# Performance work log

Measured on AMD Instinct MI355X. Metric: run time of the kernel, lower is better.

Reference implementation:

```python
import jax, jax.numpy as jnp
import numpy as np

IN_FEATURES = 4096
OUT_FEATURES = 4096
CODESZ = 4
CB_SIZE = 256


def fwht(x):
    """Fast Walsh-Hadamard transform over the last dim (power of 2), unnormalized."""
    shape = x.shape
    n = shape[-1]
    x = x.reshape(-1, n)
    h = 1
    while h < n:  # log2(n) fixed iterations
        x = x.reshape(x.shape[0], -1, 2, h)
        a = x[:, :, 0:1, :]
        b = x[:, :, 1:2, :]
        x = jnp.concatenate([a + b, a - b], axis=2)
        h *= 2
    return x.reshape(shape)


def setup_inputs() -> dict:
    key = jax.random.key(0)
    k1, k2, k3, k4, k5, k6 = jax.random.split(key, 6)
    inp = {
        "input": jax.random.normal(k1, (4, 2048, IN_FEATURES), dtype=jnp.float32),
        "SU": jax.random.uniform(k2, (IN_FEATURES,), dtype=jnp.float32),
        "SV": jax.random.uniform(k3, (OUT_FEATURES,), dtype=jnp.float32),
        "cb": jax.random.normal(k4, (CB_SIZE, CODESZ), dtype=jnp.float32),
        "Qidxs": jax.random.randint(k5, (OUT_FEATURES, IN_FEATURES // CODESZ), 0, CB_SIZE, dtype=jnp.int32),
        "Wscale": jnp.ones((1,), dtype=jnp.float32),
        "bias": jax.random.normal(k6, (OUT_FEATURES,), dtype=jnp.float32),
    }
    return inp


def reference(input, SU, SV, cb, Qidxs, Wscale, bias):
    q_in = IN_FEATURES   # power of 2 -> had_left is None, K_left = 1
    q_out = OUT_FEATURES # power of 2 -> had_right is None, K_right = 1
    x = input.reshape(-1, input.shape[-1])          # [T, in]
    x = x * SU                                       # input sign/scale vector
    # matmul_hadUt_cuda: FWHT / sqrt(n) * wscale
    x = fwht(x) * (Wscale[0] / jnp.sqrt(jnp.float32(q_in)))
    # codebook decode + matmul: W [q_out, q_in] from indices
    W = cb[Qidxs].reshape(q_out, q_in)               # gather decode
    out = jnp.einsum('ti,oi->to', x, W)              # [T, q_out]
    # matmul_hadU_cuda on the output side: FWHT / sqrt(n)
    out = fwht(out) / jnp.sqrt(jnp.float32(q_out))
    out = out[..., :OUT_FEATURES]
    out = out * SV
    out = out.reshape(*input.shape[:-1], OUT_FEATURES)
    out = out + bias
    return out
```

## Files before the change

### kernel.cpp

```cpp
#include <hip/hip_runtime.h>
#include <cstdint>


using bf16x8 = __attribute__((ext_vector_type(8))) __bf16;
using f32x4  = __attribute__((ext_vector_type(4))) float;

__device__ __forceinline__ unsigned short f2bf(float f) {
    unsigned int u = __float_as_uint(f);
    unsigned int r = (u + 0x7fffu + ((u >> 16) & 1u)) >> 16;
    return (unsigned short)r;
}

__device__ __forceinline__ void fwht4096(float* row, int t) {
    for (int h = 1; h < 4096; h <<= 1) {
#pragma unroll
        for (int q = 0; q < 8; ++q) {
            int p = t + (q << 8);
            int i = ((p & ~(h - 1)) << 1) | (p & (h - 1));
            float a = row[i];
            float b = row[i + h];
            row[i]     = a + b;
            row[i + h] = a - b;
        }
        __syncthreads();
    }
}

__global__ __launch_bounds__(256) void fwht_in_kernel(const float* __restrict__ inp,
                                                      const float* __restrict__ SU,
                                                      const float* __restrict__ wscale,
                                                      unsigned short* __restrict__ X) {
    __shared__ float row[4096];
    const int t = threadIdx.x;
    const size_t base = (size_t)blockIdx.x * 4096;
    const float4* in4 = (const float4*)(inp + base);
    const float4* su4 = (const float4*)SU;
#pragma unroll
    for (int j = 0; j < 4; ++j) {
        int v = t + (j << 8);
        float4 x = in4[v];
        float4 s = su4[v];
        x.x *= s.x; x.y *= s.y; x.z *= s.z; x.w *= s.w;
        ((float4*)row)[v] = x;
    }
    __syncthreads();
    fwht4096(row, t);
    const float sc = wscale[0] * 0.015625f;
#pragma unroll
    for (int j = 0; j < 2; ++j) {
        int i0 = (t << 3) + (j << 11);
        union { unsigned short us[8]; uint4 v4; } pk;
#pragma unroll
        for (int c = 0; c < 8; ++c) pk.us[c] = f2bf(row[i0 + c] * sc);
        *(uint4*)(X + base + i0) = pk.v4;
    }
}

__global__ __launch_bounds__(256) void decode_kernel(const int* __restrict__ Qidxs,
                                                     const float* __restrict__ cb,
                                                     unsigned short* __restrict__ Wb) {
    __shared__ float4 cbs[256];
    const int t = threadIdx.x;
    cbs[t] = ((const float4*)cb)[t];
    __syncthreads();
    const size_t o = blockIdx.x;
    const int* q = Qidxs + o * 1024;
    ushort4* wrow = (ushort4*)(Wb + o * 4096);
#pragma unroll
    for (int jj = 0; jj < 4; ++jj) {
        int j = t + (jj << 8);
        int idx = q[j];
        float4 v = cbs[idx];
        ushort4 w4;
        w4.x = f2bf(v.x); w4.y = f2bf(v.y); w4.z = f2bf(v.z); w4.w = f2bf(v.w);
        wrow[j] = w4;
    }
}


__device__ __forceinline__ void stage_part(const unsigned short* __restrict__ src,
                                           int grow, int kt,
                                           unsigned short* dst, int tid) {
#pragma unroll
    for (int j = 0; j < 2; ++j) {
        int u = tid + j * 512;
        int r = u >> 3;
        int q = (u & 7) ^ (r & 7);
        const unsigned short* g = src + (size_t)(grow + r) * 4096 + kt + q * 8;
        __builtin_amdgcn_global_load_lds(
            (const __attribute__((address_space(1))) unsigned int*)g,
            (__attribute__((address_space(3))) unsigned int*)((char*)dst + u * 16),
            16, 0, 0);
    }
}

#define VM4 asm volatile("s_waitcnt vmcnt(4)" ::: "memory")
#define VM0 asm volatile("s_waitcnt vmcnt(0)" ::: "memory")

#define PHASE(MQ, NQ, PA, PB, STAGE, VM) do {                                      \
    bf16x8 a0_[4], a1_[4], b0_[2], b1_[2];                                         \
    const char* pA_ = (const char*)(PA);                                           \
    const char* pB_ = (const char*)(PB);                                           \
    _Pragma("unroll")                                                              \
    for (int mf_ = 0; mf_ < 4; ++mf_) {                                            \
        a0_[mf_] = *(const bf16x8*)(pA_ + aRow + mf_ * 4096 + pu0);                \
        a1_[mf_] = *(const bf16x8*)(pA_ + aRow + mf_ * 4096 + pu1);                \
    }                                                                              \
    _Pragma("unroll")                                                              \
    for (int nf_ = 0; nf_ < 2; ++nf_) {                                            \
        b0_[nf_] = *(const bf16x8*)(pB_ + bRow + nf_ * 8192 + pu0);                \
        b1_[nf_] = *(const bf16x8*)(pB_ + bRow + nf_ * 8192 + pu1);                \
    }                                                                              \
    STAGE;                                                                         \
    __builtin_amdgcn_s_barrier();                                                  \
    __builtin_amdgcn_s_setprio(1);                                                 \
    _Pragma("unroll")                                                              \
    for (int mf_ = 0; mf_ < 4; ++mf_) {                                            \
        _Pragma("unroll")                                                          \
        for (int nf_ = 0; nf_ < 2; ++nf_) {                                        \
            acc[(MQ)*4 + mf_][(NQ)*2 + nf_] = __builtin_amdgcn_mfma_f32_16x16x32_bf16( \
                a0_[mf_], b0_[nf_], acc[(MQ)*4 + mf_][(NQ)*2 + nf_], 0, 0, 0);     \
            acc[(MQ)*4 + mf_][(NQ)*2 + nf_] = __builtin_amdgcn_mfma_f32_16x16x32_bf16( \
                a1_[mf_], b1_[nf_], acc[(MQ)*4 + mf_][(NQ)*2 + nf_], 0, 0, 0);     \
        }                                                                          \
    }                                                                              \
    __builtin_amdgcn_s_setprio(0);                                                 \
    VM;                                                                            \
    __builtin_amdgcn_s_barrier();                                                  \
} while (0)

__global__ __launch_bounds__(512, 2) void gemm8_kernel(const unsigned short* __restrict__ X,
                                                       const unsigned short* __restrict__ Wb,
                                                       float* __restrict__ C) {
    __shared__ unsigned short ldsA[2][2][8192];
    __shared__ unsigned short ldsB[2][2][8192];

    const int tid  = threadIdx.x;
    const int lane = tid & 63;
    const int w    = tid >> 6;
    const int wm   = w >> 2;
    const int wn   = w & 3;

    const int bid   = blockIdx.x;
    const int xcd   = bid & 7;
    const int local = bid >> 3;
    const int tm = (xcd >> 1) * 8 + (local >> 3);
    const int tn = (xcd & 1) * 8 + (local & 7);
    const int brow = tm * 256;
    const int bcol = tn * 256;

    const int lr = lane & 15;
    const int lh = lane & 7;
    const int lg = lane >> 4;
    const int aRow = (wm * 16 + lr) * 128;
    const int bRow = (wn * 16 + lr) * 128;
    const int pu0 = (lg ^ lh) * 16;
    const int pu1 = ((4 + lg) ^ lh) * 16;

    f32x4 acc[8][4] = {};

    stage_part(X,  brow,       0,  &ldsA[0][0][0], tid);
    stage_part(Wb, bcol,       0,  &ldsB[0][0][0], tid);
    stage_part(Wb, bcol + 128, 0,  &ldsB[0][1][0], tid);
    stage_part(X,  brow + 128, 0,  &ldsA[0][1][0], tid);
    stage_part(X,  brow,       64, &ldsA[1][0][0], tid);
    stage_part(Wb, bcol,       64, &ldsB[1][0][0], tid);
    VM4;
    __builtin_amdgcn_s_barrier();

    for (int i = 0; i < 31; ++i) {
        const int kt1 = i * 128 + 64;
        const int ktA = i * 128 + 128;
        const int ktB = i * 128 + 192;
        PHASE(0, 0, &ldsA[0][0][0], &ldsB[0][0][0], stage_part(Wb, bcol + 128, kt1, &ldsB[1][1][0], tid), );
        PHASE(0, 1, &ldsA[0][0][0], &ldsB[0][1][0], stage_part(X,  brow + 128, kt1, &ldsA[1][1][0], tid), );
        PHASE(1, 0, &ldsA[0][1][0], &ldsB[0][0][0], stage_part(X,  brow,       ktA, &ldsA[0][0][0], tid), );
        PHASE(1, 1, &ldsA[0][1][0], &ldsB[0][1][0], stage_part(Wb, bcol,       ktA, &ldsB[0][0][0], tid), VM4);
        PHASE(0, 0, &ldsA[1][0][0], &ldsB[1][0][0], stage_part(Wb, bcol + 128, ktA, &ldsB[0][1][0], tid), );
        PHASE(0, 1, &ldsA[1][0][0], &ldsB[1][1][0], stage_part(X,  brow + 128, ktA, &ldsA[0][1][0], tid), );
        PHASE(1, 0, &ldsA[1][1][0], &ldsB[1][0][0], stage_part(X,  brow,       ktB, &ldsA[1][0][0], tid), );
        PHASE(1, 1, &ldsA[1][1][0], &ldsB[1][1][0], stage_part(Wb, bcol,       ktB, &ldsB[1][0][0], tid), VM4);
    }
    {
        const int kt1 = 4032;
        PHASE(0, 0, &ldsA[0][0][0], &ldsB[0][0][0], stage_part(Wb, bcol + 128, kt1, &ldsB[1][1][0], tid), );
        PHASE(0, 1, &ldsA[0][0][0], &ldsB[0][1][0], stage_part(X,  brow + 128, kt1, &ldsA[1][1][0], tid), );
        PHASE(1, 0, &ldsA[0][1][0], &ldsB[0][0][0], , );
        PHASE(1, 1, &ldsA[0][1][0], &ldsB[0][1][0], , VM0);
        PHASE(0, 0, &ldsA[1][0][0], &ldsB[1][0][0], , );
        PHASE(0, 1, &ldsA[1][0][0], &ldsB[1][1][0], , );
        PHASE(1, 0, &ldsA[1][1][0], &ldsB[1][0][0], , );
        PHASE(1, 1, &ldsA[1][1][0], &ldsB[1][1][0], , );
    }

#pragma unroll
    for (int mf = 0; mf < 8; ++mf) {
        int row0 = brow + wm * 16 + mf * 32 + (lane >> 4) * 4;
#pragma unroll
        for (int nf = 0; nf < 4; ++nf) {
            int col = bcol + wn * 16 + nf * 64 + lr;
#pragma unroll
            for (int r = 0; r < 4; ++r)
                C[(size_t)(row0 + r) * 4096 + col] = acc[mf][nf][r];
        }
    }
}

__global__ __launch_bounds__(256) void fwht_out_kernel(float* __restrict__ out,
                                                       const float* __restrict__ SV,
                                                       const float* __restrict__ bias) {
    __shared__ float row[4096];
    const int t = threadIdx.x;
    const size_t base = (size_t)blockIdx.x * 4096;
    float4* o4 = (float4*)(out + base);
#pragma unroll
    for (int j = 0; j < 4; ++j) {
        int v = t + (j << 8);
        ((float4*)row)[v] = o4[v];
    }
    __syncthreads();
    fwht4096(row, t);
    const float4* sv4 = (const float4*)SV;
    const float4* b4  = (const float4*)bias;
#pragma unroll
    for (int j = 0; j < 4; ++j) {
        int v = t + (j << 8);
        float4 x = ((float4*)row)[v];
        float4 s = sv4[v];
        float4 b = b4[v];
        x.x = x.x * (s.x * 0.015625f) + b.x;
        x.y = x.y * (s.y * 0.015625f) + b.y;
        x.z = x.z * (s.z * 0.015625f) + b.z;
        x.w = x.w * (s.w * 0.015625f) + b.w;
        o4[v] = x;
    }
}

extern "C" void kernel_launch(void* const* d_in, const int* in_sizes, int n_in,
                              void* d_out, int out_size, void* d_ws, size_t ws_size,
                              hipStream_t stream) {
    const float* inp    = (const float*)d_in[0];
    const float* SU     = (const float*)d_in[1];
    const float* SV     = (const float*)d_in[2];
    const float* cb     = (const float*)d_in[3];
    const int*   Qidxs  = (const int*)d_in[4];
    const float* Wscale = (const float*)d_in[5];
    const float* bias   = (const float*)d_in[6];
    float* out = (float*)d_out;

    unsigned short* X  = (unsigned short*)d_ws;
    unsigned short* Wb = (unsigned short*)((char*)d_ws + (size_t)8192 * 4096 * 2);

    hipLaunchKernelGGL(fwht_in_kernel, dim3(8192), dim3(256), 0, stream, inp, SU, Wscale, X);
    hipLaunchKernelGGL(decode_kernel,  dim3(4096), dim3(256), 0, stream, Qidxs, cb, Wb);
    hipLaunchKernelGGL(gemm8_kernel,   dim3(512),  dim3(512), 0, stream, X, Wb, out);
    hipLaunchKernelGGL(fwht_out_kernel, dim3(8192), dim3(256), 0, stream, out, SV, bias);
}
```

Measured before the change: 612.4 us.

## Use register radix-16 FWHT with XOR-swizzled LDS and reuse fragments in GEMM

Both FWHT kernels move from 12 barrier-separated radix-2 passes over shared memory to three radix-16 passes. Each pass does a 16-point transform in registers, using an XOR-swizzled layout so the strided accesses avoid bank conflicts. This removes most barriers and shared-memory traffic. The GEMM main loop is also restructured to load A and B fragments once per k-subtile and reuse them across the four quadrant MFMA groups in a snake order, cutting LDS reads at the cost of extra live registers.

```diff
diff --git a/kernel.cpp b/kernel.cpp
--- a/kernel.cpp
+++ b/kernel.cpp
@@ -11,48 +11,81 @@
     return (unsigned short)r;
 }
 
-__device__ __forceinline__ void fwht4096(float* row, int t) {
-    for (int h = 1; h < 4096; h <<= 1) {
-#pragma unroll
-        for (int q = 0; q < 8; ++q) {
-            int p = t + (q << 8);
-            int i = ((p & ~(h - 1)) << 1) | (p & (h - 1));
-            float a = row[i];
-            float b = row[i + h];
-            row[i]     = a + b;
-            row[i + h] = a - b;
+__device__ __forceinline__ void h16(float v[16]) {
+#pragma unroll
+    for (int h = 1; h < 16; h <<= 1) {
+#pragma unroll
+        for (int g = 0; g < 16; g += (h << 1)) {
+#pragma unroll
+            for (int k = g; k < g + h; ++k) {
+                float x = v[k], y = v[k + h];
+                v[k] = x + y; v[k + h] = x - y;
+            }
         }
-        __syncthreads();
-    }
-}
+    }
+}
+
 
 __global__ __launch_bounds__(256) void fwht_in_kernel(const float* __restrict__ inp,
                                                       const float* __restrict__ SU,
                                                       const float* __restrict__ wscale,
                                                       unsigned short* __restrict__ X) {
-    __shared__ float row[4096];
+    __shared__ float s[4096];
     const int t = threadIdx.x;
     const size_t base = (size_t)blockIdx.x * 4096;
     const float4* in4 = (const float4*)(inp + base);
     const float4* su4 = (const float4*)SU;
 #pragma unroll
     for (int j = 0; j < 4; ++j) {
-        int v = t + (j << 8);
+        const int v = t + (j << 8);
         float4 x = in4[v];
-        float4 s = su4[v];
-        x.x *= s.x; x.y *= s.y; x.z *= s.z; x.w *= s.w;
-        ((float4*)row)[v] = x;
-    }
-    __syncthreads();
-    fwht4096(row, t);
+        float4 u = su4[v];
+        x.x *= u.x; x.y *= u.y; x.z *= u.z; x.w *= u.w;
+        const int a = v >> 6, b = (v >> 2) & 15, c0 = (v & 3) << 2;
+        float* row = s + a * 256 + ((b ^ a) << 4);
+        row[(c0 + 0) ^ b] = x.x; row[(c0 + 1) ^ b] = x.y;
+        row[(c0 + 2) ^ b] = x.z; row[(c0 + 3) ^ b] = x.w;
+    }
+    __syncthreads();
+    float v[16];
+    {
+        const int a = t >> 4, b = t & 15;
+        float* row = s + a * 256 + ((b ^ a) << 4);
+#pragma unroll
+        for (int c = 0; c < 16; ++c) v[c] = row[c ^ b];
+        h16(v);
+#pragma unroll
+        for (int c = 0; c < 16; ++c) row[c ^ b] = v[c];
+    }
+    __syncthreads();
+    {
+        const int a = t >> 4, c = t & 15;
+#pragma unroll
+        for (int b = 0; b < 16; ++b) v[b] = s[a * 256 + ((b ^ a) << 4) + (c ^ b)];
+        h16(v);
+#pragma unroll
+        for (int b = 0; b < 16; ++b) s[a * 256 + ((b ^ a) << 4) + (c ^ b)] = v[b];
+    }
+    __syncthreads();
+    {
+        const int b = t >> 4, c = t & 15;
+#pragma unroll
+        for (int a = 0; a < 16; ++a) v[a] = s[a * 256 + ((b ^ a) << 4) + (c ^ b)];
+        h16(v);
+#pragma unroll
+        for (int a = 0; a < 16; ++a) s[a * 256 + ((b ^ a) << 4) + (c ^ b)] = v[a];
+    }
+    __syncthreads();
     const float sc = wscale[0] * 0.015625f;
 #pragma unroll
-    for (int j = 0; j < 2; ++j) {
-        int i0 = (t << 3) + (j << 11);
-        union { unsigned short us[8]; uint4 v4; } pk;
-#pragma unroll
-        for (int c = 0; c < 8; ++c) pk.us[c] = f2bf(row[i0 + c] * sc);
-        *(uint4*)(X + base + i0) = pk.v4;
+    for (int p = 0; p < 2; ++p) {
+        const int i0 = (p << 11) + (t << 3);
+        const int a = i0 >> 8, b = (i0 >> 4) & 15, c0 = i0 & 15;
+        const float* row = s + a * 256 + ((b ^ a) << 4);
+        union { unsigned short us[8]; uint4 q; } pk;
+#pragma unroll
+        for (int z = 0; z < 8; ++z) pk.us[z] = f2bf(row[(c0 + z) ^ b] * sc);
+        *(uint4*)(X + base + i0) = pk.q;
     }
 }
 
@@ -97,36 +130,42 @@
 #define VM4 asm volatile("s_waitcnt vmcnt(4)" ::: "memory")
 #define VM0 asm volatile("s_waitcnt vmcnt(0)" ::: "memory")
 
-#define PHASE(MQ, NQ, PA, PB, STAGE, VM) do {                                      \
-    bf16x8 a0_[4], a1_[4], b0_[2], b1_[2];                                         \
+#define RD_A(HOFF) do { _Pragma("unroll")                                          \
+    for (int m_ = 0; m_ < 4; ++m_) {                                               \
+        Ak0[m_] = *(const bf16x8*)(pA_ + (HOFF) + aRow + m_ * 4096 + pu0);         \
+        Ak1[m_] = *(const bf16x8*)(pA_ + (HOFF) + aRow + m_ * 4096 + pu1);         \
+    } } while (0)
+
+#define RD_B(D0, D1, HOFF) do { _Pragma("unroll")                                  \
+    for (int n_ = 0; n_ < 2; ++n_) {                                               \
+        D0[n_] = *(const bf16x8*)(pB_ + (HOFF) + bRow + n_ * 8192 + pu0);          \
+        D1[n_] = *(const bf16x8*)(pB_ + (HOFF) + bRow + n_ * 8192 + pu1);          \
+    } } while (0)
+
+#define MMQ(MQ, NQ, Bk0, Bk1) do {                                                 \
+    __builtin_amdgcn_s_setprio(1);                                                 \
+    _Pragma("unroll")                                                              \
+    for (int m_ = 0; m_ < 4; ++m_) { _Pragma("unroll")                             \
+        for (int n_ = 0; n_ < 2; ++n_) {                                           \
+            acc[(MQ)*4+m_][(NQ)*2+n_] = __builtin_amdgcn_mfma_f32_16x16x32_bf16(   \
+                Ak0[m_], Bk0[n_], acc[(MQ)*4+m_][(NQ)*2+n_], 0, 0, 0);             \
+            acc[(MQ)*4+m_][(NQ)*2+n_] = __builtin_amdgcn_mfma_f32_16x16x32_bf16(   \
+                Ak1[m_], Bk1[n_], acc[(MQ)*4+m_][(NQ)*2+n_], 0, 0, 0);             \
+        } }                                                                        \
+    __builtin_amdgcn_s_setprio(0); } while (0)
+
+#define KTILE(PA, PB, ST1, ST2, ST3, ST4, VM_) do {                                \
     const char* pA_ = (const char*)(PA);                                           \
     const char* pB_ = (const char*)(PB);                                           \
-    _Pragma("unroll")                                                              \
-    for (int mf_ = 0; mf_ < 4; ++mf_) {                                            \
-        a0_[mf_] = *(const bf16x8*)(pA_ + aRow + mf_ * 4096 + pu0);                \
-        a1_[mf_] = *(const bf16x8*)(pA_ + aRow + mf_ * 4096 + pu1);                \
-    }                                                                              \
-    _Pragma("unroll")                                                              \
-    for (int nf_ = 0; nf_ < 2; ++nf_) {                                            \
-        b0_[nf_] = *(const bf16x8*)(pB_ + bRow + nf_ * 8192 + pu0);                \
-        b1_[nf_] = *(const bf16x8*)(pB_ + bRow + nf_ * 8192 + pu1);                \
-    }                                                                              \
-    STAGE;                                                                         \
-    __builtin_amdgcn_s_barrier();                                                  \
-    __builtin_amdgcn_s_setprio(1);                                                 \
-    _Pragma("unroll")                                                              \
-    for (int mf_ = 0; mf_ < 4; ++mf_) {                                            \
-        _Pragma("unroll")                                                          \
-        for (int nf_ = 0; nf_ < 2; ++nf_) {                                        \
-            acc[(MQ)*4 + mf_][(NQ)*2 + nf_] = __builtin_amdgcn_mfma_f32_16x16x32_bf16( \
-                a0_[mf_], b0_[nf_], acc[(MQ)*4 + mf_][(NQ)*2 + nf_], 0, 0, 0);     \
-            acc[(MQ)*4 + mf_][(NQ)*2 + nf_] = __builtin_amdgcn_mfma_f32_16x16x32_bf16( \
-                a1_[mf_], b1_[nf_], acc[(MQ)*4 + mf_][(NQ)*2 + nf_], 0, 0, 0);     \
-        }                                                                          \
-    }                                                                              \
-    __builtin_amdgcn_s_setprio(0);                                                 \
-    VM;                                                                            \
-    __builtin_amdgcn_s_barrier();                                                  \
+    bf16x8 Ak0[4], Ak1[4], B0k0[2], B0k1[2], B1k0[2], B1k1[2];                     \
+    RD_A(0); RD_B(B0k0, B0k1, 0); ST1; __builtin_amdgcn_s_barrier();               \
+    MMQ(0, 0, B0k0, B0k1); __builtin_amdgcn_s_barrier();                           \
+    RD_B(B1k0, B1k1, 16384); ST2; __builtin_amdgcn_s_barrier();                    \
+    MMQ(0, 1, B1k0, B1k1); __builtin_amdgcn_s_barrier();                           \
+    RD_A(16384); ST3; __builtin_amdgcn_s_barrier();                                \
+    MMQ(1, 1, B1k0, B1k1); __builtin_amdgcn_s_barrier();                           \
+    ST4; __builtin_amdgcn_s_barrier();                                             \
+    MMQ(1, 0, B0k0, B0k1); VM_; __builtin_amdgcn_s_barrier();                      \
 } while (0)
 
 __global__ __launch_bounds__(512, 2) void gemm8_kernel(const unsigned short* __restrict__ X,
@@ -172,25 +211,24 @@
         const int kt1 = i * 128 + 64;
         const int ktA = i * 128 + 128;
         const int ktB = i * 128 + 192;
-        PHASE(0, 0, &ldsA[0][0][0], &ldsB[0][0][0], stage_part(Wb, bcol + 128, kt1, &ldsB[1][1][0], tid), );
-        PHASE(0, 1, &ldsA[0][0][0], &ldsB[0][1][0], stage_part(X,  brow + 128, kt1, &ldsA[1][1][0], tid), );
-        PHASE(1, 0, &ldsA[0][1][0], &ldsB[0][0][0], stage_part(X,  brow,       ktA, &ldsA[0][0][0], tid), );
-        PHASE(1, 1, &ldsA[0][1][0], &ldsB[0][1][0], stage_part(Wb, bcol,       ktA, &ldsB[0][0][0], tid), VM4);
-        PHASE(0, 0, &ldsA[1][0][0], &ldsB[1][0][0], stage_part(Wb, bcol + 128, ktA, &ldsB[0][1][0], tid), );
-        PHASE(0, 1, &ldsA[1][0][0], &ldsB[1][1][0], stage_part(X,  brow + 128, ktA, &ldsA[0][1][0], tid), );
-        PHASE(1, 0, &ldsA[1][1][0], &ldsB[1][0][0], stage_part(X,  brow,       ktB, &ldsA[1][0][0], tid), );
-        PHASE(1, 1, &ldsA[1][1][0], &ldsB[1][1][0], stage_part(Wb, bcol,       ktB, &ldsB[1][0][0], tid), VM4);
-    }
-    {
-        const int kt1 = 4032;
-        PHASE(0, 0, &ldsA[0][0][0], &ldsB[0][0][0], stage_part(Wb, bcol + 128, kt1, &ldsB[1][1][0], tid), );
-        PHASE(0, 1, &ldsA[0][0][0], &ldsB[0][1][0], stage_part(X,  brow + 128, kt1, &ldsA[1][1][0], tid), );
-        PHASE(1, 0, &ldsA[0][1][0], &ldsB[0][0][0], , );
-        PHASE(1, 1, &ldsA[0][1][0], &ldsB[0][1][0], , VM0);
-        PHASE(0, 0, &ldsA[1][0][0], &ldsB[1][0][0], , );
-        PHASE(0, 1, &ldsA[1][0][0], &ldsB[1][1][0], , );
-        PHASE(1, 0, &ldsA[1][1][0], &ldsB[1][0][0], , );
-        PHASE(1, 1, &ldsA[1][1][0], &ldsB[1][1][0], , );
+        KTILE(&ldsA[0][0][0], &ldsB[0][0][0],
+              stage_part(Wb, bcol + 128, kt1, &ldsB[1][1][0], tid),
+              stage_part(X,  brow + 128, kt1, &ldsA[1][1][0], tid),
+              stage_part(X,  brow,       ktA, &ldsA[0][0][0], tid),
+              stage_part(Wb, bcol,       ktA, &ldsB[0][0][0], tid), VM4);
+        KTILE(&ldsA[1][0][0], &ldsB[1][0][0],
+              stage_part(Wb, bcol + 128, ktA, &ldsB[0][1][0], tid),
+              stage_part(X,  brow + 128, ktA, &ldsA[0][1][0], tid),
+              stage_part(X,  brow,       ktB, &ldsA[1][0][0], tid),
+              stage_part(Wb, bcol,       ktB, &ldsB[1][0][0], tid), VM4);
+    }
+    {
+        const int kt1 = 31 * 128 + 64;
+        KTILE(&ldsA[0][0][0], &ldsB[0][0][0],
+              stage_part(Wb, bcol + 128, kt1, &ldsB[1][1][0], tid),
+              stage_part(X,  brow + 128, kt1, &ldsA[1][1][0], tid),
+              , , VM0);
+        KTILE(&ldsA[1][0][0], &ldsB[1][0][0], , , , , );
     }
 
 #pragma unroll
@@ -209,30 +247,65 @@
 __global__ __launch_bounds__(256) void fwht_out_kernel(float* __restrict__ out,
                                                        const float* __restrict__ SV,
                                                        const float* __restrict__ bias) {
-    __shared__ float row[4096];
+    __shared__ float s[4096];
     const int t = threadIdx.x;
     const size_t base = (size_t)blockIdx.x * 4096;
     float4* o4 = (float4*)(out + base);
 #pragma unroll
     for (int j = 0; j < 4; ++j) {
-        int v = t + (j << 8);
-        ((float4*)row)[v] = o4[v];
-    }
-    __syncthreads();
-    fwht4096(row, t);
+        const int v = t + (j << 8);
+        float4 x = o4[v];
+        const int a = v >> 6, b = (v >> 2) & 15, c0 = (v & 3) << 2;
+        float* row = s + a * 256 + ((b ^ a) << 4);
+        row[(c0 + 0) ^ b] = x.x; row[(c0 + 1) ^ b] = x.y;
+        row[(c0 + 2) ^ b] = x.z; row[(c0 + 3) ^ b] = x.w;
+    }
+    __syncthreads();
+    float v[16];
+    {
+        const int a = t >> 4, b = t & 15;
+        float* row = s + a * 256 + ((b ^ a) << 4);
+#pragma unroll
+        for (int c = 0; c < 16; ++c) v[c] = row[c ^ b];
+        h16(v);
+#pragma unroll
+        for (int c = 0; c < 16; ++c) row[c ^ b] = v[c];
+    }
+    __syncthreads();
+    {
+        const int a = t >> 4, c = t & 15;
+#pragma unroll
+        for (int b = 0; b < 16; ++b) v[b] = s[a * 256 + ((b ^ a) << 4) + (c ^ b)];
+        h16(v);
+#pragma unroll
+        for (int b = 0; b < 16; ++b) s[a * 256 + ((b ^ a) << 4) + (c ^ b)] = v[b];
+    }
+    __syncthreads();
+    {
+        const int b = t >> 4, c = t & 15;
+#pragma unroll
+        for (int a = 0; a < 16; ++a) v[a] = s[a * 256 + ((b ^ a) << 4) + (c ^ b)];
+        h16(v);
+#pragma unroll
+        for (int a = 0; a < 16; ++a) s[a * 256 + ((b ^ a) << 4) + (c ^ b)] = v[a];
+    }
+    __syncthreads();
     const float4* sv4 = (const float4*)SV;
     const float4* b4  = (const float4*)bias;
 #pragma unroll
     for (int j = 0; j < 4; ++j) {
-        int v = t + (j << 8);
-        float4 x = ((float4*)row)[v];
-        float4 s = sv4[v];
-        float4 b = b4[v];
-        x.x = x.x * (s.x * 0.015625f) + b.x;
-        x.y = x.y * (s.y * 0.015625f) + b.y;
-        x.z = x.z * (s.z * 0.015625f) + b.z;
-        x.w = x.w * (s.w * 0.015625f) + b.w;
-        o4[v] = x;
+        const int vv = t + (j << 8);
+        const int a = vv >> 6, b = (vv >> 2) & 15, c0 = (vv & 3) << 2;
+        const float* row = s + a * 256 + ((b ^ a) << 4);
+        float4 x;
+        x.x = row[(c0 + 0) ^ b]; x.y = row[(c0 + 1) ^ b];
+        x.z = row[(c0 + 2) ^ b]; x.w = row[(c0 + 3) ^ b];
+        float4 sv = sv4[vv], bb = b4[vv];
+        x.x = x.x * (sv.x * 0.015625f) + bb.x;
+        x.y = x.y * (sv.y * 0.015625f) + bb.y;
+        x.z = x.z * (sv.z * 0.015625f) + bb.z;
+        x.w = x.w * (sv.w * 0.015625f) + bb.w;
+        o4[vv] = x;
     }
 }
 
```

Measured after the change: 507.1 us. -17.2%, faster.
